# Performance work log

Hardware: AMD Instinct MI355X
Metric: run time of the kernel (lower is better)

Reference implementation:

```python
import jax, jax.numpy as jnp
import numpy as np
import math

B, N, D = 4, 2048, 512
H, DH = 8, 128
INNER = H * DH


def setup_inputs() -> dict:
    key = jax.random.key(0)
    k1, k2, k3, k4 = jax.random.split(key, 4)
    x = jax.random.normal(k1, (B, N, D), dtype=jnp.float32)
    Wg = jax.random.normal(k2, (D, INNER), dtype=jnp.float32) * (1.0 / math.sqrt(D))
    Wout = jax.random.normal(k3, (INNER, D), dtype=jnp.float32) * (1.0 / math.sqrt(INNER))
    sigma = jax.random.uniform(k4, (1, H, 1, 1), dtype=jnp.float32, minval=0.5, maxval=2.5)
    return {"x": x, "Wg": Wg, "Wout": Wout, "sigma": sigma}


def reference(x, Wg, Wout, sigma):
    b, n, d = x.shape
    h, dh = H, DH
    # value projection: [b,n,d] @ [d, h*dh] -> [b,h,n,dh]
    v = (x @ Wg).reshape(b, n, h, dh).transpose(0, 2, 1, 3)
    # fixed Gaussian positional mask, shared across batch: build once per head
    pos = jnp.arange(1, n + 1, dtype=jnp.float32)
    diffs = jnp.abs(pos[:, None] - pos[None, :])  # [n, n]
    sig = sigma.reshape(h, 1, 1)  # [h,1,1]
    inv_norm = 1.0 / (jnp.sqrt(2.0 * jnp.float32(math.pi)) * sig)
    gauss = inv_norm * jnp.exp(-(diffs[None] ** 2) / (2.0 * sig ** 2))  # [h,n,n]
    corr = gauss / gauss.sum(-1, keepdims=True)  # row-normalized [h,n,n]
    # attention: broadcast mask over batch
    attn = jnp.einsum('hnm,bhmd->bhnd', corr, v)
    out = attn.transpose(0, 2, 1, 3).reshape(b, n, h * dh)
    return out @ Wout  # dropout p=0.0 -> identity
```

## Files before the change

kernel.cpp:

```cpp
#include <hip/hip_runtime.h>
#include <hip/hip_bf16.h>
#include <math.h>

#define B_ 4
#define N_ 2048
#define D_ 512
#define H_ 8
#define DH_ 128
#define INNER_ 1024
#define W_ 32
#define M_ (B_ * N_)

typedef __attribute__((ext_vector_type(8))) short short8;
typedef __attribute__((ext_vector_type(4))) float floatx4;

typedef const __attribute__((address_space(1))) char* gcp;
typedef __attribute__((address_space(3))) char* lcp;

__device__ __forceinline__ float bf16hi_to_f(unsigned u) {
    union { unsigned u; float f; } c; c.u = u; return c.f;
}
__device__ __forceinline__ unsigned f_to_bf16bits(float f) {
    union { float f; unsigned u; } c; c.f = f;
    return (c.u + 0x7fffu + ((c.u >> 16) & 1u)) >> 16;
}

struct bf16x4s { __hip_bfloat16 a, b, c, d; };

__global__ __launch_bounds__(256, 4) void g1_blur(
    const __hip_bfloat16* __restrict__ x_bf,
    const __hip_bfloat16* __restrict__ Wg_t,
    const float* __restrict__ sigma,
    __hip_bfloat16* __restrict__ attn)
{
    __shared__ char smem[33824];
    __hip_bfloat16* Asm = (__hip_bfloat16*)smem;
    __hip_bfloat16* Bsm = (__hip_bfloat16*)(smem + 16384);

    const int tid  = threadIdx.x;
    const int lane = tid & 63;
    const int w    = tid >> 6;
    const int wm   = w >> 1;
    const int wn   = w & 1;
    const int quad = lane >> 4;
    const int cl   = lane & 15;
    const int bm   = blockIdx.x;
    const int h    = blockIdx.y;
    const int n0   = bm * 64;
    const int nb0  = n0 & (N_ - 1);

    floatx4 acc[4][4];
    #pragma unroll
    for (int i = 0; i < 4; ++i)
        #pragma unroll
        for (int j = 0; j < 4; ++j) acc[i][j] = (floatx4){0.f, 0.f, 0.f, 0.f};

    const char* Ab = (const char*)x_bf;
    const char* Bb = (const char*)(Wg_t + (size_t)(h * DH_) * D_);

    for (int k0 = 0; k0 < D_; k0 += 64) {
        #pragma unroll
        for (int it = 0; it < 4; ++it) {
            int o = it * 4096 + tid * 16;
            int r = o >> 7;
            int s = (o >> 4) & 7;
            int c = s ^ (r & 7);
            int gr = n0 - W_ + r;
            gr = gr < 0 ? 0 : (gr > M_ - 1 ? M_ - 1 : gr);
            __builtin_amdgcn_global_load_lds(
                (gcp)(Ab + (size_t)gr * 1024 + k0 * 2 + c * 16), (lcp)(smem + o), 16, 0, 0);
            __builtin_amdgcn_global_load_lds(
                (gcp)(Bb + (size_t)r * 1024 + k0 * 2 + c * 16), (lcp)(smem + 16384 + o), 16, 0, 0);
        }
        __syncthreads();

        const short* As = (const short*)Asm;
        const short* Bs = (const short*)Bsm;
        #pragma unroll
        for (int kk = 0; kk < 2; ++kk) {
            short8 af[4], bf[4];
            int ch = kk * 4 + quad;
            #pragma unroll
            for (int t = 0; t < 4; ++t) {
                int ra = wm * 64 + t * 16 + cl;
                int rb = wn * 64 + t * 16 + cl;
                af[t] = *(const short8*)(As + ra * 64 + ((ch ^ (ra & 7)) * 8));
                bf[t] = *(const short8*)(Bs + rb * 64 + ((ch ^ (rb & 7)) * 8));
            }
            #pragma unroll
            for (int i = 0; i < 4; ++i)
                #pragma unroll
                for (int j = 0; j < 4; ++j)
                    acc[i][j] = __builtin_amdgcn_mfma_f32_16x16x32_bf16(
                        af[i], bf[j], acc[i][j], 0, 0, 0);
        }
        __syncthreads();
    }

    unsigned short* vsp = (unsigned short*)smem;
    float* wtab = (float*)(smem + 33280);
    float* winv = (float*)(smem + 33280 + 272);

    #pragma unroll
    for (int i = 0; i < 4; ++i) {
        #pragma unroll
        for (int jp = 0; jp < 2; ++jp) {
            #pragma unroll
            for (int rr = 0; rr < 4; ++rr) {
                int srow = wm * 64 + i * 16 + quad * 4 + rr;
                int vb = nb0 - W_ + srow;
                unsigned u = 0u;
                if (vb >= 0 && vb < N_) {
                    unsigned lo = f_to_bf16bits(acc[i][jp * 2][rr]);
                    unsigned hi = f_to_bf16bits(acc[i][jp * 2 + 1][rr]);
                    u = lo | (hi << 16);
                }
                int scol = wn * 64 + jp * 32 + cl * 2;
                *(unsigned*)(vsp + srow * 130 + scol) = u;
            }
        }
    }
    if (tid <= 2 * W_) {
        float sig = sigma[h];
        float d = (float)(tid - W_);
        wtab[tid] = __expf(-d * d / (2.0f * sig * sig));
    }
    __syncthreads();

    if (tid < 64) {
        int nbl = nb0 + tid;
        float ws = 0.f;
        #pragma unroll
        for (int j = 0; j <= 2 * W_; ++j) {
            int m = nbl - W_ + j;
            ws += (m >= 0 && m < N_) ? wtab[j] : 0.f;
        }
        winv[tid] = 1.0f / ws;
    }

    const int cg = tid & 31;
    const int rg = tid >> 5;

    float4 bacc[8];
    #pragma unroll
    for (int r = 0; r < 8; ++r) bacc[r] = make_float4(0.f, 0.f, 0.f, 0.f);
    float wreg[8] = {0.f, 0.f, 0.f, 0.f, 0.f, 0.f, 0.f, 0.f};

    const unsigned* vrow0 = (const unsigned*)(vsp + rg * 8 * 130 + cg * 4);

    #pragma unroll 8
    for (int l = 0; l < 2 * W_ + 8; ++l) {
        wreg[l & 7] = (l <= 2 * W_) ? wtab[l] : 0.f;
        const unsigned* p = vrow0 + (size_t)l * 65;
        unsigned r0 = p[0], r1 = p[1];
        float4 vv;
        vv.x = bf16hi_to_f(r0 << 16);
        vv.y = bf16hi_to_f(r0 & 0xffff0000u);
        vv.z = bf16hi_to_f(r1 << 16);
        vv.w = bf16hi_to_f(r1 & 0xffff0000u);
        #pragma unroll
        for (int r = 0; r < 8; ++r) {
            float wgt = wreg[(l - r) & 7];
            bacc[r].x += wgt * vv.x; bacc[r].y += wgt * vv.y;
            bacc[r].z += wgt * vv.z; bacc[r].w += wgt * vv.w;
        }
    }
    __syncthreads();

    #pragma unroll
    for (int r = 0; r < 8; ++r) {
        int o = rg * 8 + r;
        float s = winv[o];
        bf16x4s ov = { __float2bfloat16(bacc[r].x * s), __float2bfloat16(bacc[r].y * s),
                       __float2bfloat16(bacc[r].z * s), __float2bfloat16(bacc[r].w * s) };
        *(bf16x4s*)(attn + (size_t)(n0 + o) * INNER_ + h * DH_ + cg * 4) = ov;
    }
}

template <typename OutT>
__global__ __launch_bounds__(256, 4) void gemm_bf16_dbuf(
    const __hip_bfloat16* __restrict__ A, const __hip_bfloat16* __restrict__ Bt,
    OutT* __restrict__ C, int M, int N, int K)
{
    __shared__ char smem[32768];

    const int tid  = threadIdx.x;
    const int lane = tid & 63;
    const int w    = tid >> 6;
    const int wm   = w >> 1;
    const int wn   = w & 1;
    const int bm   = blockIdx.y;
    const int bn   = blockIdx.x;

    const int kh = lane >> 4;
    const int ml = lane & 15;

    floatx4 acc[2][2];
    #pragma unroll
    for (int i = 0; i < 2; ++i)
        #pragma unroll
        for (int j = 0; j < 2; ++j) acc[i][j] = (floatx4){0.f, 0.f, 0.f, 0.f};

    const char* Ab = (const char*)(A + (size_t)(bm * 64) * K);
    const char* Bb = (const char*)(Bt + (size_t)(bn * 64) * K);
    const size_t rowstride = (size_t)K * 2;

    auto issue = [&](int buf, int k0) {
        #pragma unroll
        for (int it = 0; it < 2; ++it) {
            int o = it * 4096 + tid * 16;
            int r = o >> 7;
            int s = (o >> 4) & 7;
            int c = s ^ (r & 7);
            size_t goff = (size_t)r * rowstride + (size_t)k0 * 2 + c * 16;
            __builtin_amdgcn_global_load_lds((gcp)(Ab + goff),
                (lcp)(smem + buf * 16384 + o), 16, 0, 0);
            __builtin_amdgcn_global_load_lds((gcp)(Bb + goff),
                (lcp)(smem + buf * 16384 + 8192 + o), 16, 0, 0);
        }
    };
    auto consume = [&](int buf) {
        const short* As = (const short*)(smem + buf * 16384);
        const short* Bs = (const short*)(smem + buf * 16384 + 8192);
        short8 af[2][2], bf[2][2];
        #pragma unroll
        for (int t = 0; t < 2; ++t) {
            int ra = wm * 32 + t * 16 + ml;
            int rb = wn * 32 + t * 16 + ml;
            #pragma unroll
            for (int kk = 0; kk < 2; ++kk) {
                int ch = kk * 4 + kh;
                af[t][kk] = *(const short8*)(As + ra * 64 + ((ch ^ (ra & 7)) * 8));
                bf[t][kk] = *(const short8*)(Bs + rb * 64 + ((ch ^ (rb & 7)) * 8));
            }
        }
        #pragma unroll
        for (int kk = 0; kk < 2; ++kk)
            #pragma unroll
            for (int i = 0; i < 2; ++i)
                #pragma unroll
                for (int j = 0; j < 2; ++j)
                    acc[i][j] = __builtin_amdgcn_mfma_f32_16x16x32_bf16(
                        af[i][kk], bf[j][kk], acc[i][j], 0, 0, 0);
    };

    const int nk = K >> 6;
    issue(0, 0);
    for (int kt = 0; kt < nk; kt += 2) {
        __syncthreads();
        if (kt + 1 < nk) issue(1, (kt + 1) << 6);
        consume(0);
        __syncthreads();
        if (kt + 2 < nk) issue(0, (kt + 2) << 6);
        consume(1);
    }
    __syncthreads();

    float* Cs = (float*)smem;
    const int rq = lane >> 4;
    const int cl = lane & 15;
    #pragma unroll
    for (int i = 0; i < 2; ++i)
        #pragma unroll
        for (int j = 0; j < 2; ++j)
            #pragma unroll
            for (int r = 0; r < 4; ++r)
                Cs[(wm * 32 + i * 16 + rq * 4 + r) * 64 + wn * 32 + j * 16 + cl] = acc[i][j][r];
    __syncthreads();

    if constexpr (sizeof(OutT) == 2) {
        #pragma unroll
        for (int p = 0; p < 2; ++p) {
            int idx = p * 256 + tid;
            int rr = idx >> 3;
            int cc = (idx & 7) * 8;
            const float* src = Cs + rr * 64 + cc;
            __hip_bfloat16 o[8];
            #pragma unroll
            for (int e = 0; e < 8; ++e) o[e] = __float2bfloat16(src[e]);
            *(short8*)((__hip_bfloat16*)C + (size_t)(bm * 64 + rr) * N + bn * 64 + cc) = *(short8*)o;
        }
    } else {
        #pragma unroll
        for (int p = 0; p < 4; ++p) {
            int idx = p * 256 + tid;
            int rr = idx >> 4;
            int cc = (idx & 15) * 4;
            float4 vv = *(const float4*)(Cs + rr * 64 + cc);
            *(float4*)((float*)C + (size_t)(bm * 64 + rr) * N + bn * 64 + cc) = vv;
        }
    }
}

template <bool PERM>
__device__ __forceinline__ void transpose32p(
    const float* __restrict__ src, __hip_bfloat16* __restrict__ dst,
    int R, int Cn, int rt, int ct, int tid)
{
    __shared__ float t[32][33];
    int c0 = ct * 32, r0 = rt * 32;
    int lx = tid & 31, ly = tid >> 5;
    #pragma unroll
    for (int i = 0; i < 32; i += 8)
        t[ly + i][lx] = src[(size_t)(r0 + ly + i) * Cn + c0 + lx];
    __syncthreads();
    int colx = PERM ? (r0 + ((lx & 15) * 2 | (lx >> 4))) : (r0 + lx);
    #pragma unroll
    for (int i = 0; i < 32; i += 8)
        dst[(size_t)(c0 + ly + i) * R + colx] = __float2bfloat16(t[lx][ly + i]);
}

__global__ __launch_bounds__(256) void prep(
    const float* __restrict__ x, const float* __restrict__ Wg,
    const float* __restrict__ Wout, __hip_bfloat16* __restrict__ x_bf,
    __hip_bfloat16* __restrict__ Wg_t, __hip_bfloat16* __restrict__ Wout_t)
{
    const int bid = blockIdx.x;
    const int tid = threadIdx.x;
    if (bid < 2048) {
        int i = bid * 256 + tid;
        const float4* s = (const float4*)x + (size_t)i * 2;
        float4 a = s[0], b = s[1];
        __hip_bfloat16 o[8] = {
            __float2bfloat16(a.x), __float2bfloat16(a.y), __float2bfloat16(a.z), __float2bfloat16(a.w),
            __float2bfloat16(b.x), __float2bfloat16(b.y), __float2bfloat16(b.z), __float2bfloat16(b.w)};
        *(short8*)(x_bf + (size_t)i * 8) = *(short8*)o;
    } else if (bid < 2560) {
        int id2 = bid - 2048;
        transpose32p<false>(Wg, Wg_t, D_, INNER_, id2 >> 5, id2 & 31, tid);
    } else {
        int id2 = bid - 2560;
        transpose32p<true>(Wout, Wout_t, INNER_, D_, id2 >> 4, id2 & 15, tid);
    }
}

extern "C" void kernel_launch(void* const* d_in, const int* in_sizes, int n_in,
                              void* d_out, int out_size, void* d_ws, size_t ws_size,
                              hipStream_t stream) {
    const float* x     = (const float*)d_in[0];
    const float* Wg    = (const float*)d_in[1];
    const float* Wout  = (const float*)d_in[2];
    const float* sigma = (const float*)d_in[3];
    float* out = (float*)d_out;

    char* ws = (char*)d_ws;
    __hip_bfloat16* x_bf   = (__hip_bfloat16*)ws;
    __hip_bfloat16* Wg_t   = (__hip_bfloat16*)(ws + (((size_t)8)  << 20));
    __hip_bfloat16* Wout_t = (__hip_bfloat16*)(ws + (((size_t)9)  << 20));
    __hip_bfloat16* attn   = (__hip_bfloat16*)(ws + (((size_t)10) << 20));

    prep<<<dim3(3072), dim3(256), 0, stream>>>(x, Wg, Wout, x_bf, Wg_t, Wout_t);

    g1_blur<<<dim3(M_ / 64, H_), dim3(256), 0, stream>>>(x_bf, Wg_t, sigma, attn);

    gemm_bf16_dbuf<float><<<dim3(D_ / 64, M_ / 64), dim3(256), 0, stream>>>(
        attn, Wout_t, out, M_, D_, INNER_);
}
```

Measured before the change: 130.2 us.

## Compute banded Gaussian blur with MFMA using a Toeplitz weight fragment

Replaces the scalar FMA sliding-window blur over the V tile with bf16 MFMA instructions. A Toeplitz band matrix is built from a bf16 weight table, and V is stored transposed in shared memory so it can serve as the B operand. The Wout column permutation in prep is dropped, since channel order now matches directly. This moves blur arithmetic onto the matrix cores, at the cost of rounding the weights to bf16, doing redundant MACs on zero band entries, and issuing scalar bf16 output stores.

```diff
diff --git a/kernel.cpp b/kernel.cpp
--- a/kernel.cpp
+++ b/kernel.cpp
@@ -17,15 +17,15 @@
 typedef const __attribute__((address_space(1))) char* gcp;
 typedef __attribute__((address_space(3))) char* lcp;
 
-__device__ __forceinline__ float bf16hi_to_f(unsigned u) {
-    union { unsigned u; float f; } c; c.u = u; return c.f;
-}
 __device__ __forceinline__ unsigned f_to_bf16bits(float f) {
     union { float f; unsigned u; } c; c.f = f;
     return (c.u + 0x7fffu + ((c.u >> 16) & 1u)) >> 16;
 }
-
-struct bf16x4s { __hip_bfloat16 a, b, c, d; };
+__device__ __forceinline__ float bf16s_to_f(unsigned short s) {
+    union { unsigned u; float f; } c; c.u = ((unsigned)s) << 16; return c.f;
+}
+
+#define VST 136
 
 __global__ __launch_bounds__(256, 4) void g1_blur(
     const __hip_bfloat16* __restrict__ x_bf,
@@ -33,7 +33,7 @@
     const float* __restrict__ sigma,
     __hip_bfloat16* __restrict__ attn)
 {
-    __shared__ char smem[33824];
+    __shared__ char smem[35328];
     __hip_bfloat16* Asm = (__hip_bfloat16*)smem;
     __hip_bfloat16* Bsm = (__hip_bfloat16*)(smem + 16384);
 
@@ -97,83 +97,102 @@
         __syncthreads();
     }
 
-    unsigned short* vsp = (unsigned short*)smem;
-    float* wtab = (float*)(smem + 33280);
-    float* winv = (float*)(smem + 33280 + 272);
+    unsigned short* vsT   = (unsigned short*)smem;
+    unsigned short* wtabS = (unsigned short*)(smem + 34816);
+    float*          winv  = (float*)(smem + 35072);
 
     #pragma unroll
     for (int i = 0; i < 4; ++i) {
         #pragma unroll
-        for (int jp = 0; jp < 2; ++jp) {
+        for (int j = 0; j < 4; ++j) {
+            int ch   = wn * 64 + j * 16 + cl;
+            int row0 = wm * 64 + i * 16 + quad * 4;
+            unsigned p01 = 0u, p23 = 0u;
             #pragma unroll
             for (int rr = 0; rr < 4; ++rr) {
-                int srow = wm * 64 + i * 16 + quad * 4 + rr;
-                int vb = nb0 - W_ + srow;
-                unsigned u = 0u;
-                if (vb >= 0 && vb < N_) {
-                    unsigned lo = f_to_bf16bits(acc[i][jp * 2][rr]);
-                    unsigned hi = f_to_bf16bits(acc[i][jp * 2 + 1][rr]);
-                    u = lo | (hi << 16);
-                }
-                int scol = wn * 64 + jp * 32 + cl * 2;
-                *(unsigned*)(vsp + srow * 130 + scol) = u;
-            }
+                int vb = nb0 - W_ + row0 + rr;
+                unsigned bits = (vb >= 0 && vb < N_) ? f_to_bf16bits(acc[i][j][rr]) : 0u;
+                if (rr < 2) p01 |= bits << (rr * 16);
+                else        p23 |= bits << ((rr - 2) * 16);
+            }
+            unsigned* dst = (unsigned*)(vsT + ch * VST + row0);
+            dst[0] = p01; dst[1] = p23;
         }
     }
     if (tid <= 2 * W_) {
         float sig = sigma[h];
         float d = (float)(tid - W_);
-        wtab[tid] = __expf(-d * d / (2.0f * sig * sig));
+        wtabS[tid] = (unsigned short)f_to_bf16bits(__expf(-d * d / (2.0f * sig * sig)));
     }
     __syncthreads();
 
     if (tid < 64) {
-        int nbl = nb0 + tid;
         float ws = 0.f;
         #pragma unroll
-        for (int j = 0; j <= 2 * W_; ++j) {
-            int m = nbl - W_ + j;
-            ws += (m >= 0 && m < N_) ? wtab[j] : 0.f;
+        for (int l = 0; l <= 2 * W_; ++l) {
+            int vb = nb0 + tid + l - W_;
+            ws += (vb >= 0 && vb < N_) ? bf16s_to_f(wtabS[l]) : 0.f;
         }
         winv[tid] = 1.0f / ws;
     }
 
-    const int cg = tid & 31;
-    const int rg = tid >> 5;
-
-    float4 bacc[8];
-    #pragma unroll
-    for (int r = 0; r < 8; ++r) bacc[r] = make_float4(0.f, 0.f, 0.f, 0.f);
-    float wreg[8] = {0.f, 0.f, 0.f, 0.f, 0.f, 0.f, 0.f, 0.f};
-
-    const unsigned* vrow0 = (const unsigned*)(vsp + rg * 8 * 130 + cg * 4);
-
-    #pragma unroll 8
-    for (int l = 0; l < 2 * W_ + 8; ++l) {
-        wreg[l & 7] = (l <= 2 * W_) ? wtab[l] : 0.f;
-        const unsigned* p = vrow0 + (size_t)l * 65;
-        unsigned r0 = p[0], r1 = p[1];
-        float4 vv;
-        vv.x = bf16hi_to_f(r0 << 16);
-        vv.y = bf16hi_to_f(r0 & 0xffff0000u);
-        vv.z = bf16hi_to_f(r1 << 16);
-        vv.w = bf16hi_to_f(r1 & 0xffff0000u);
-        #pragma unroll
-        for (int r = 0; r < 8; ++r) {
-            float wgt = wreg[(l - r) & 7];
-            bacc[r].x += wgt * vv.x; bacc[r].y += wgt * vv.y;
-            bacc[r].z += wgt * vv.z; bacc[r].w += wgt * vv.w;
-        }
-    }
-    __syncthreads();
-
-    #pragma unroll
-    for (int r = 0; r < 8; ++r) {
-        int o = rg * 8 + r;
-        float s = winv[o];
-        bf16x4s ov = { __float2bfloat16(bacc[r].x * s), __float2bfloat16(bacc[r].y * s),
-                       __float2bfloat16(bacc[r].z * s), __float2bfloat16(bacc[r].w * s) };
-        *(bf16x4s*)(attn + (size_t)(n0 + o) * INNER_ + h * DH_ + cg * 4) = ov;
+    short afr[2][4][8];
+    #pragma unroll
+    for (int mi = 0; mi < 2; ++mi) {
+        int row = wm * 32 + mi * 16 + cl;
+        #pragma unroll
+        for (int k4 = 0; k4 < 4; ++k4) {
+            int lb = k4 * 32 + quad * 8 - row;
+            #pragma unroll
+            for (int j = 0; j < 8; ++j) {
+                int l = lb + j;
+                afr[mi][k4][j] = (l >= 0 && l <= 2 * W_) ? (short)wtabS[l] : (short)0;
+            }
+        }
+    }
+    __syncthreads();
+
+    floatx4 oacc[2][4];
+    #pragma unroll
+    for (int mi = 0; mi < 2; ++mi)
+        #pragma unroll
+        for (int ni = 0; ni < 4; ++ni) oacc[mi][ni] = (floatx4){0.f, 0.f, 0.f, 0.f};
+
+    #pragma unroll
+    for (int k4 = 0; k4 < 4; ++k4) {
+        short8 bfr[4];
+        #pragma unroll
+        for (int ni = 0; ni < 4; ++ni) {
+            int ch = wn * 64 + ni * 16 + cl;
+            bfr[ni] = *(const short8*)((const short*)vsT + ch * VST + k4 * 32 + quad * 8);
+        }
+        #pragma unroll
+        for (int mi = 0; mi < 2; ++mi)
+            #pragma unroll
+            for (int ni = 0; ni < 4; ++ni)
+                oacc[mi][ni] = __builtin_amdgcn_mfma_f32_16x16x32_bf16(
+                    *(short8*)afr[mi][k4], bfr[ni], oacc[mi][ni], 0, 0, 0);
+    }
+
+    float wv[2][4];
+    #pragma unroll
+    for (int mi = 0; mi < 2; ++mi)
+        #pragma unroll
+        for (int r = 0; r < 4; ++r)
+            wv[mi][r] = winv[wm * 32 + mi * 16 + quad * 4 + r];
+
+    #pragma unroll
+    for (int mi = 0; mi < 2; ++mi) {
+        #pragma unroll
+        for (int ni = 0; ni < 4; ++ni) {
+            int ch = wn * 64 + ni * 16 + cl;
+            #pragma unroll
+            for (int r = 0; r < 4; ++r) {
+                int orow = wm * 32 + mi * 16 + quad * 4 + r;
+                attn[(size_t)(n0 + orow) * INNER_ + h * DH_ + ch] =
+                    __float2bfloat16(oacc[mi][ni][r] * wv[mi][r]);
+            }
+        }
     }
 }
 
@@ -292,8 +311,7 @@
     }
 }
 
-template <bool PERM>
-__device__ __forceinline__ void transpose32p(
+__device__ __forceinline__ void transpose32(
     const float* __restrict__ src, __hip_bfloat16* __restrict__ dst,
     int R, int Cn, int rt, int ct, int tid)
 {
@@ -304,10 +322,9 @@
     for (int i = 0; i < 32; i += 8)
         t[ly + i][lx] = src[(size_t)(r0 + ly + i) * Cn + c0 + lx];
     __syncthreads();
-    int colx = PERM ? (r0 + ((lx & 15) * 2 | (lx >> 4))) : (r0 + lx);
     #pragma unroll
     for (int i = 0; i < 32; i += 8)
-        dst[(size_t)(c0 + ly + i) * R + colx] = __float2bfloat16(t[lx][ly + i]);
+        dst[(size_t)(c0 + ly + i) * R + r0 + lx] = __float2bfloat16(t[lx][ly + i]);
 }
 
 __global__ __launch_bounds__(256) void prep(
@@ -327,10 +344,10 @@
         *(short8*)(x_bf + (size_t)i * 8) = *(short8*)o;
     } else if (bid < 2560) {
         int id2 = bid - 2048;
-        transpose32p<false>(Wg, Wg_t, D_, INNER_, id2 >> 5, id2 & 31, tid);
+        transpose32(Wg, Wg_t, D_, INNER_, id2 >> 5, id2 & 31, tid);
     } else {
         int id2 = bid - 2560;
-        transpose32p<true>(Wout, Wout_t, INNER_, D_, id2 >> 4, id2 & 15, tid);
+        transpose32(Wout, Wout_t, INNER_, D_, id2 >> 4, id2 & 15, tid);
     }
 }
 
```

Result: faster. 118.8 us (-8.7%).
